# Optimization experiments

Hardware: AMD Instinct MI355X
Metric: run time of the kernel (lower is better)

Reference implementation:

```python
import jax, jax.numpy as jnp
import numpy as np

N = 100000   # nodes
E = 400000   # edges
B = 4000     # graphs
D = 300      # emb_dim
L = 5        # num_layer
MAX_LEN = 50 # max_atom_num (hard-coded in forward)
SELF_LOOP_BOND_TYPE = 4
BN_EPS = 1e-5


def setup_inputs() -> dict:
    key = jax.random.key(0)
    ks = jax.random.split(key, 12)
    x = jax.random.randint(ks[0], (N, 2), 0, 3)            # col0 atom type (<120), col1 chirality (<3)
    edge_index = jax.random.randint(ks[1], (2, E), 0, N)
    edge_attr = jax.random.randint(ks[2], (E, 2), 0, 3)    # col0 bond type (<6), col1 direction (<3)
    batch = jnp.sort(jax.random.randint(ks[3], (N,), 0, B))
    sc = 0.05
    x_emb1 = jax.random.normal(ks[4], (120, D)) * sc
    x_emb2 = jax.random.normal(ks[5], (3, D)) * sc
    e_emb1 = jax.random.normal(ks[6], (L, 6, D)) * sc
    e_emb2 = jax.random.normal(ks[7], (L, 3, D)) * sc
    W1 = jax.random.normal(ks[8], (L, D, 2 * D)) * (1.0 / np.sqrt(D))
    b1 = jnp.zeros((L, 2 * D))
    W2 = jax.random.normal(ks[9], (L, 2 * D, D)) * (1.0 / np.sqrt(2 * D))
    b2 = jnp.zeros((L, D))
    bn_gamma = jnp.ones((L, D))
    bn_beta = jnp.zeros((L, D))
    return dict(x=x, edge_index=edge_index, edge_attr=edge_attr, batch=batch,
                num_graphs=B, x_emb1=x_emb1, x_emb2=x_emb2, e_emb1=e_emb1,
                e_emb2=e_emb2, W1=W1, b1=b1, W2=W2, b2=b2,
                bn_gamma=bn_gamma, bn_beta=bn_beta)


def reference(x, edge_index, edge_attr, batch, num_graphs,
              x_emb1, x_emb2, e_emb1, e_emb2, W1, b1, W2, b2, bn_gamma, bn_beta):
    n = x.shape[0]
    # input node embedding: atom type + chirality
    h = x_emb1[x[:, 0]] + x_emb2[x[:, 1]]  # [N, D]
    # add self loops (bond_type=4, direction=0)
    loop = jnp.arange(n)
    src = jnp.concatenate([edge_index[0], loop])
    dst = jnp.concatenate([edge_index[1], loop])
    ea0 = jnp.concatenate([edge_attr[:, 0], jnp.full((n,), SELF_LOOP_BOND_TYPE, edge_attr.dtype)])
    ea1 = jnp.concatenate([edge_attr[:, 1], jnp.zeros((n,), edge_attr.dtype)])
    num_layers = W1.shape[0]
    for l in range(num_layers):
        ee = e_emb1[l][ea0] + e_emb2[l][ea1]                 # [E+N, D] edge embeddings
        msg = h[src] + ee                                     # gather + message
        agg = jax.ops.segment_sum(msg, dst, num_segments=n)   # scatter-add aggregation
        hid = jax.nn.relu(agg @ W1[l] + b1[l])                # GIN MLP
        h2 = hid @ W2[l] + b2[l]
        mean = h2.mean(axis=0)                                # BatchNorm1d (batch stats, biased var)
        var = jnp.mean((h2 - mean) ** 2, axis=0)
        h2 = (h2 - mean) * jax.lax.rsqrt(var + BN_EPS) * bn_gamma[l] + bn_beta[l]
        # dropout with drop_ratio=0 is identity; relu on all but last layer
        h = h2 if l == num_layers - 1 else jax.nn.relu(h2)
    # global mean pool over graphs
    counts = jax.ops.segment_sum(jnp.ones((n,), h.dtype), batch, num_segments=num_graphs)
    pooled = jax.ops.segment_sum(h, batch, num_segments=num_graphs) / jnp.maximum(counts, 1.0)[:, None]
    # atom_feature_pad: pad per-graph node features to MAX_LEN with mask
    idx = jnp.arange(n)
    is_start = jnp.concatenate([jnp.array([True]), batch[1:] != batch[:-1]])
    start = jax.lax.cummax(jnp.where(is_start, idx, 0))
    pos = idx - start                                          # position within each graph
    valid = pos < MAX_LEN
    posc = jnp.minimum(pos, MAX_LEN - 1)
    d = h.shape[1]
    node_feature = jnp.zeros((num_graphs, MAX_LEN, d), h.dtype).at[batch, posc].add(
        h * valid[:, None].astype(h.dtype))
    mask = jnp.zeros((num_graphs, MAX_LEN), h.dtype).at[batch, posc].add(valid.astype(h.dtype))
    return pooled, node_feature, mask
```

## Files before the change

### kernel.cpp

```cpp
#include <hip/hip_runtime.h>
#include <cstdint>

#define D 300
#define MAXLEN 50
#define K1P 320
#define H1 600
#define H1P 608
#define W1ROWS 640
#define W2ROWS 384

typedef __attribute__((ext_vector_type(8))) short s16x8;
typedef __attribute__((ext_vector_type(4))) short s16x4;
typedef __attribute__((ext_vector_type(4))) float f32x4;
typedef __attribute__((ext_vector_type(2))) float f32x2;
typedef __attribute__((ext_vector_type(4))) int i32x4;

__device__ __forceinline__ unsigned short f2b(float f) {
  uint32_t u = __builtin_bit_cast(uint32_t, f);
  u += 0x7FFFu + ((u >> 16) & 1u);
  return (unsigned short)(u >> 16);
}
__device__ __forceinline__ float b2f(unsigned short s) {
  return __builtin_bit_cast(float, (uint32_t)s << 16);
}
__device__ __forceinline__ void gld_lds16(const void* g, void* l) {
  __builtin_amdgcn_global_load_lds((const __attribute__((address_space(1))) void*)g,
                                   (__attribute__((address_space(3))) void*)l, 16, 0, 0);
}

__global__ void k_cmb(const float* __restrict__ xe1, const float* __restrict__ xe2,
                      unsigned short* __restrict__ cmb, int total ) {
  int i = blockIdx.x * blockDim.x + threadIdx.x;
  if (i >= total) return;
  int c = i / 75, d = (i - c * 75) * 4;
  int a = c / 3, b = c - a * 3;
  s16x4 out;
#pragma unroll
  for (int j = 0; j < 4; ++j) out[j] = (short)f2b(xe1[(size_t)a * D + d + j] + xe2[(size_t)b * D + d + j]);
  *(s16x4*)(cmb + (size_t)c * K1P + d) = out;
}

__global__ void k_cid(const int* __restrict__ x, int* __restrict__ cid, int N) {
  int i = blockIdx.x * blockDim.x + threadIdx.x;
  if (i < N) cid[i] = x[2 * i] * 3 + x[2 * i + 1];
}

__global__ void k_count(const int* __restrict__ key, int* __restrict__ cnt, int n) {
  int i = blockIdx.x * blockDim.x + threadIdx.x;
  if (i < n) atomicAdd(&cnt[key[i]], 1);
}

__global__ void k_scan1(const int* __restrict__ in, int* __restrict__ part, int n) {
  __shared__ int red[256];
  int tid = threadIdx.x;
  int base = blockIdx.x * 1024 + tid * 4;
  i32x4 v = {0, 0, 0, 0};
  if (base + 3 < n) v = *(const i32x4*)(in + base);
  else {
#pragma unroll
    for (int k = 0; k < 4; ++k) v[k] = (base + k < n) ? in[base + k] : 0;
  }
  int s = v[0] + v[1] + v[2] + v[3];
  red[tid] = s;
  __syncthreads();
  for (int off = 1; off < 256; off <<= 1) {
    int t = (tid >= off) ? red[tid - off] : 0;
    __syncthreads();
    red[tid] += t;
    __syncthreads();
  }
  if (tid == 255) part[blockIdx.x] = red[255];
}

__global__ void k_scan2(int* __restrict__ part, int P) {
  __shared__ int sm[1024];
  int tid = threadIdx.x;
  int v = (tid < P) ? part[tid] : 0;
  sm[tid] = v;
  __syncthreads();
  for (int off = 1; off < 1024; off <<= 1) {
    int t = (tid >= off) ? sm[tid - off] : 0;
    __syncthreads();
    sm[tid] += t;
    __syncthreads();
  }
  if (tid < P) part[tid] = sm[tid] - v;
  if (tid == 1023) part[P] = sm[1023];
}

__global__ void k_scan3(const int* __restrict__ in, const int* __restrict__ part,
                        int* __restrict__ out, int n, int P) {
  __shared__ int red[256];
  int tid = threadIdx.x;
  int base = blockIdx.x * 1024 + tid * 4;
  i32x4 v = {0, 0, 0, 0};
  if (base + 3 < n) v = *(const i32x4*)(in + base);
  else {
#pragma unroll
    for (int k = 0; k < 4; ++k) v[k] = (base + k < n) ? in[base + k] : 0;
  }
  int s = v[0] + v[1] + v[2] + v[3];
  red[tid] = s;
  __syncthreads();
  for (int off = 1; off < 256; off <<= 1) {
    int t = (tid >= off) ? red[tid - off] : 0;
    __syncthreads();
    red[tid] += t;
    __syncthreads();
  }
  int pre = red[tid] - s + part[blockIdx.x];
  if (base < n) out[base] = pre;
  if (base + 1 < n) out[base + 1] = pre + v[0];
  if (base + 2 < n) out[base + 2] = pre + v[0] + v[1];
  if (base + 3 < n) out[base + 3] = pre + v[0] + v[1] + v[2];
  if (blockIdx.x == 0 && tid == 0) out[n] = part[P];
}

__global__ void k_fill(const int* __restrict__ src, const int* __restrict__ dst,
                       const int* __restrict__ ea, const int* __restrict__ cid,
                       int* __restrict__ cur, const int* __restrict__ offs,
                       int* __restrict__ ssrc, int* __restrict__ scid,
                       int* __restrict__ cnt18, int E_) {
  int e = blockIdx.x * blockDim.x + threadIdx.x;
  if (e >= E_) return;
  int d = dst[e];
  int s = src[e];
  int p = atomicAdd(&cur[d], 1);
  int pos = offs[d] + p;
  ssrc[pos] = s;
  scid[pos] = cid[s];
  int co = ea[2 * e] * 3 + ea[2 * e + 1];
  atomicAdd(&cnt18[d * 18 + co], 1);
}

__global__ void k_cnt18bf(const int* __restrict__ cnt18, unsigned short* __restrict__ aggbf, int N) {
  int idx = blockIdx.x * blockDim.x + threadIdx.x;
  if (idx >= N * 10) return;
  int i = idx / 10, j = idx - i * 10;
  uint32_t o = 0;
  if (j < 9) {
    int c0 = cnt18[i * 18 + 2 * j] + (2 * j == 12 ? 1 : 0);
    int c1 = cnt18[i * 18 + 2 * j + 1];
    o = (uint32_t)f2b((float)c0) | ((uint32_t)f2b((float)c1) << 16);
  }
  *(uint32_t*)(aggbf + (size_t)i * K1P + D + j * 2) = o;
}

__global__ void k_ecw1(const float* __restrict__ ee1, const float* __restrict__ ee2,
                       const float* __restrict__ W1, unsigned short* __restrict__ W1tA,
                       int L_, int total ) {
  int idx = blockIdx.x * blockDim.x + threadIdx.x;
  if (idx >= total) return;
  int k18 = idx % 18;
  int n = (idx / 18) % H1;
  int l = idx / (18 * H1);
  const float* e1 = ee1 + ((size_t)l * 6 + k18 / 3) * D;
  const float* e2 = ee2 + ((size_t)l * 3 + k18 % 3) * D;
  const float* w = W1 + (size_t)l * D * H1 + n;
  float s = 0.f;
  for (int d = 0; d < D; ++d) s += (e1[d] + e2[d]) * w[(size_t)d * H1];
  W1tA[(size_t)l * W1ROWS * K1P + (size_t)n * K1P + D + k18] = f2b(s);
}

template <int FUSE>
__global__ void k_agg(const unsigned short* __restrict__ hin, const int* __restrict__ ridx,
                      const int* __restrict__ offs, const float* __restrict__ scale,
                      const float* __restrict__ shift, const int* __restrict__ selfcid,
                      unsigned short* __restrict__ aggbf, int N) {
  int w = (int)((blockIdx.x * blockDim.x + threadIdx.x) >> 6);
  if (w >= N) return;
  int lane = threadIdx.x & 63;
  float sc0[3], sc1[3], sh0[3], sh1[3];
#pragma unroll
  for (int i = 0; i < 3; ++i) {
    int d2 = i * 64 + lane;
    if (FUSE && d2 < 150) {
      f32x2 s = *(const f32x2*)(scale + d2 * 2);
      f32x2 t = *(const f32x2*)(shift + d2 * 2);
      sc0[i] = s[0]; sc1[i] = s[1]; sh0[i] = t[0]; sh1[i] = t[1];
    } else { sc0[i] = sc1[i] = sh0[i] = sh1[i] = 0.f; }
  }
  int beg = offs[w], end = offs[w + 1];
  int wrow = FUSE ? w : selfcid[w];
  float s0[3], s1[3];
#pragma unroll
  for (int i = 0; i < 3; ++i) {
    int d2 = i * 64 + lane;
    float a = 0.f, b = 0.f;
    if (d2 < 150) {
      uint32_t u = *(const uint32_t*)(hin + (size_t)wrow * K1P + d2 * 2);
      a = b2f((unsigned short)(u & 0xFFFF));
      b = b2f((unsigned short)(u >> 16));
      if (FUSE) { a = fmaxf(a * sc0[i] + sh0[i], 0.f); b = fmaxf(b * sc1[i] + sh1[i], 0.f); }
    }
    s0[i] = a; s1[i] = b;
  }
  int j = beg;
  for (; j + 4 <= end; j += 4) {
    int sv0 = ridx[j], sv1 = ridx[j + 1], sv2 = ridx[j + 2], sv3 = ridx[j + 3];
    const unsigned short* p0 = hin + (size_t)sv0 * K1P;
    const unsigned short* p1 = hin + (size_t)sv1 * K1P;
    const unsigned short* p2 = hin + (size_t)sv2 * K1P;
    const unsigned short* p3 = hin + (size_t)sv3 * K1P;
#pragma unroll
    for (int i = 0; i < 3; ++i) {
      int d2 = i * 64 + lane;
      if (d2 < 150) {
        uint32_t u0 = *(const uint32_t*)(p0 + d2 * 2);
        uint32_t u1 = *(const uint32_t*)(p1 + d2 * 2);
        uint32_t u2 = *(const uint32_t*)(p2 + d2 * 2);
        uint32_t u3 = *(const uint32_t*)(p3 + d2 * 2);
        float a0 = b2f((unsigned short)(u0 & 0xFFFF)), b0 = b2f((unsigned short)(u0 >> 16));
        float a1 = b2f((unsigned short)(u1 & 0xFFFF)), b1 = b2f((unsigned short)(u1 >> 16));
        float a2 = b2f((unsigned short)(u2 & 0xFFFF)), b2 = b2f((unsigned short)(u2 >> 16));
        float a3 = b2f((unsigned short)(u3 & 0xFFFF)), b3 = b2f((unsigned short)(u3 >> 16));
        if (FUSE) {
          a0 = fmaxf(a0 * sc0[i] + sh0[i], 0.f); b0 = fmaxf(b0 * sc1[i] + sh1[i], 0.f);
          a1 = fmaxf(a1 * sc0[i] + sh0[i], 0.f); b1 = fmaxf(b1 * sc1[i] + sh1[i], 0.f);
          a2 = fmaxf(a2 * sc0[i] + sh0[i], 0.f); b2 = fmaxf(b2 * sc1[i] + sh1[i], 0.f);
          a3 = fmaxf(a3 * sc0[i] + sh0[i], 0.f); b3 = fmaxf(b3 * sc1[i] + sh1[i], 0.f);
        }
        s0[i] += (a0 + a1) + (a2 + a3);
        s1[i] += (b0 + b1) + (b2 + b3);
      }
    }
  }
  for (; j < end; ++j) {
    int sv = ridx[j];
    const unsigned short* rp = hin + (size_t)sv * K1P;
#pragma unroll
    for (int i = 0; i < 3; ++i) {
      int d2 = i * 64 + lane;
      if (d2 < 150) {
        uint32_t u = *(const uint32_t*)(rp + d2 * 2);
        float a = b2f((unsigned short)(u & 0xFFFF)), b = b2f((unsigned short)(u >> 16));
        if (FUSE) { a = fmaxf(a * sc0[i] + sh0[i], 0.f); b = fmaxf(b * sc1[i] + sh1[i], 0.f); }
        s0[i] += a;
        s1[i] += b;
      }
    }
  }
#pragma unroll
  for (int i = 0; i < 3; ++i) {
    int d2 = i * 64 + lane;
    if (d2 < 150) {
      uint32_t o = (uint32_t)f2b(s0[i]) | ((uint32_t)f2b(s1[i]) << 16);
      *(uint32_t*)(aggbf + (size_t)w * K1P + d2 * 2) = o;
    }
  }
}

__global__ void k_wconv(const float* __restrict__ W, unsigned short* __restrict__ Wt,
                        int K, int Nout, int Kp, int total) {
  int idx = blockIdx.x * blockDim.x + threadIdx.x;
  if (idx >= total) return;
  int n = idx / Kp, k = idx - n * Kp;
  float v = (k < K && n < Nout) ? W[(size_t)k * Nout + n] : 0.f;
  Wt[idx] = f2b(v);
}

template <int K, int EPI>
__global__ __launch_bounds__(256, 3) void k_gemm(
    const unsigned short* __restrict__ A, const unsigned short* __restrict__ Bt,
    const float* __restrict__ bias, unsigned short* __restrict__ Cb,
    float* __restrict__ sums, int M, int Nout, int ldc, int CT) {
  constexpr int T = K / 32;
  __shared__ __align__(16) unsigned short smem[24576];

  int nwg = gridDim.x;
  int q = nwg >> 3, r8 = nwg & 7;
  int xcd = blockIdx.x & 7, oidx = blockIdx.x >> 3;
  int wid = (xcd < r8 ? xcd * (q + 1) : r8 * (q + 1) + (xcd - r8) * q) + oidx;
  int ct = wid % CT, rt = wid / CT;
  const int rowBase = rt * 128, colBase = ct * 128;

  const int tid = threadIdx.x, lane = tid & 63, wave = tid >> 6;
  const int wm = wave >> 1, wn = wave & 1;
  const int l15 = lane & 15, lg = lane >> 4;

  unsigned short* Asm = smem;
  unsigned short* Bsm = smem + 12288;

  auto stage = [&](int s, int t) {
#pragma unroll
    for (int i = 0; i < 2; ++i) {
      int u = tid + i * 256;
      int rr = u >> 2;
      int cdat = (u & 3) ^ ((rr >> 1) & 3);
      int gr = rowBase + rr; if (gr >= M) gr = M - 1;
      gld_lds16(A + (size_t)gr * K + t * 32 + cdat * 8, Asm + s * 4096 + u * 8);
      gld_lds16(Bt + (size_t)(colBase + rr) * K + t * 32 + cdat * 8, Bsm + s * 4096 + u * 8);
    }
  };

  f32x4 acc[4][4] = {};
  stage(0, 0);
  stage(1, 1);
#pragma unroll
  for (int t = 0; t < T; ++t) {
    if (t + 1 < T) asm volatile("s_waitcnt vmcnt(4)" ::: "memory");
    else           asm volatile("s_waitcnt vmcnt(0)" ::: "memory");
    __builtin_amdgcn_s_barrier();
    __builtin_amdgcn_sched_barrier(0);
    const unsigned short* bA = Asm + (t % 3) * 4096;
    const unsigned short* bB = Bsm + (t % 3) * 4096;
    s16x8 af[4], bf[4];
#pragma unroll
    for (int i = 0; i < 4; ++i) {
      int ra = wm * 64 + i * 16 + l15;
      int rb = wn * 64 + i * 16 + l15;
      af[i] = *(const s16x8*)(bA + ((size_t)ra * 4 + (lg ^ ((ra >> 1) & 3))) * 8);
      bf[i] = *(const s16x8*)(bB + ((size_t)rb * 4 + (lg ^ ((rb >> 1) & 3))) * 8);
    }
    if (t + 2 < T) stage((t + 2) % 3, t + 2);
#pragma unroll
    for (int mi = 0; mi < 4; ++mi)
#pragma unroll
      for (int ni = 0; ni < 4; ++ni)
        acc[mi][ni] = __builtin_amdgcn_mfma_f32_16x16x32_bf16(af[mi], bf[ni], acc[mi][ni], 0, 0, 0);
  }

  float bnS[4] = {0.f, 0.f, 0.f, 0.f}, bnQ[4] = {0.f, 0.f, 0.f, 0.f};
#pragma unroll
  for (int ni = 0; ni < 4; ++ni) {
    int col = colBase + wn * 64 + ni * 16 + l15;
    if (col >= (EPI ? ldc : Nout)) continue;
    bool inN = col < Nout;
    float bv = inN ? bias[col] : 0.f;
#pragma unroll
    for (int mi = 0; mi < 4; ++mi) {
      int row0 = rowBase + wm * 64 + mi * 16 + lg * 4;
#pragma unroll
      for (int rr = 0; rr < 4; ++rr) {
        int row = row0 + rr;
        if (row < M) {
          float v = inN ? acc[mi][ni][rr] + bv : 0.f;
          if (EPI) v = fmaxf(v, 0.f);
          else { bnS[ni] += v; bnQ[ni] += v * v; }
          Cb[(size_t)row * ldc + col] = f2b(v);
        }
      }
    }
  }
  if (!EPI) {
#pragma unroll
    for (int ni = 0; ni < 4; ++ni) {
      float cs = bnS[ni], cq = bnQ[ni];
      cs += __shfl_xor(cs, 16); cq += __shfl_xor(cq, 16);
      cs += __shfl_xor(cs, 32); cq += __shfl_xor(cq, 32);
      int col = colBase + wn * 64 + ni * 16 + l15;
      if (lg == 0 && col < Nout) {
        atomicAdd(&sums[col], cs);
        atomicAdd(&sums[D + col], cq);
      }
    }
  }
}

__global__ void k_bnfinal(const float* __restrict__ sums, const float* __restrict__ sumsq,
                          const float* __restrict__ gamma, const float* __restrict__ beta,
                          float* __restrict__ scale, float* __restrict__ shift, int N) {
  int c = threadIdx.x;
  if (c >= D) return;
  float inv = 1.f / (float)N;
  float mean = sums[c] * inv;
  float var = sumsq[c] * inv - mean * mean;
  if (var < 0.f) var = 0.f;
  float sc = gamma[c] * rsqrtf(var + 1e-5f);
  scale[c] = sc;
  shift[c] = beta[c] - mean * sc;
}

__global__ void k_pool(const unsigned short* __restrict__ hb, const float* __restrict__ scale,
                       const float* __restrict__ shift, const int* __restrict__ gs,
                       const int* __restrict__ gc, float* __restrict__ pooled, int total ) {
  int gid = blockIdx.x * blockDim.x + threadIdx.x;
  if (gid >= total) return;
  int g = gid / 75, c4 = (gid - g * 75) * 4;
  int start = gs[g], cnt = gc[g];
  f32x4 s = {0.f, 0.f, 0.f, 0.f};
  for (int i = 0; i < cnt; ++i) {
    s16x4 in = *(const s16x4*)(hb + (size_t)(start + i) * K1P + c4);
#pragma unroll
    for (int j = 0; j < 4; ++j) s[j] += b2f((unsigned short)in[j]);
  }
  f32x4 sc = *(const f32x4*)(scale + c4);
  f32x4 sh = *(const f32x4*)(shift + c4);
  float dv = (cnt > 0) ? (float)cnt : 1.f;
  f32x4 out;
#pragma unroll
  for (int j = 0; j < 4; ++j) out[j] = (s[j] * sc[j] + sh[j] * (float)cnt) / dv;
  *(f32x4*)(pooled + (size_t)g * D + c4) = out;
}

__global__ void k_nf(const unsigned short* __restrict__ hb, const float* __restrict__ scale,
                     const float* __restrict__ shift, const int* __restrict__ gs,
                     const int* __restrict__ gc, float* __restrict__ nf, float* __restrict__ mask) {
  int g = blockIdx.x;
  int start = gs[g], cnt = gc[g];
  int lim = cnt < MAXLEN ? cnt : MAXLEN;
  for (int idx = threadIdx.x; idx < MAXLEN * 75; idx += 256) {
    int p = idx / 75;
    int c4 = (idx - p * 75) * 4;
    f32x4 v = {0.f, 0.f, 0.f, 0.f};
    if (p < lim) {
      s16x4 in = *(const s16x4*)(hb + (size_t)(start + p) * K1P + c4);
      f32x4 sc = *(const f32x4*)(scale + c4);
      f32x4 sh = *(const f32x4*)(shift + c4);
#pragma unroll
      for (int j = 0; j < 4; ++j) v[j] = b2f((unsigned short)in[j]) * sc[j] + sh[j];
    }
    *(f32x4*)(nf + (size_t)g * (MAXLEN * D) + p * D + c4) = v;
  }
  if (threadIdx.x < MAXLEN) mask[(size_t)g * MAXLEN + threadIdx.x] = (threadIdx.x < lim) ? 1.f : 0.f;
}

extern "C" void kernel_launch(void* const* d_in, const int* in_sizes, int n_in,
                              void* d_out, int out_size, void* d_ws, size_t ws_size,
                              hipStream_t stream) {
  const int* x      = (const int*)d_in[0];
  const int* ei     = (const int*)d_in[1];
  const int* ea     = (const int*)d_in[2];
  const int* batch  = (const int*)d_in[3];
  const float* xe1  = (const float*)d_in[5];
  const float* xe2  = (const float*)d_in[6];
  const float* ee1  = (const float*)d_in[7];
  const float* ee2  = (const float*)d_in[8];
  const float* W1   = (const float*)d_in[9];
  const float* b1   = (const float*)d_in[10];
  const float* W2   = (const float*)d_in[11];
  const float* b2   = (const float*)d_in[12];
  const float* gamma = (const float*)d_in[13];
  const float* beta  = (const float*)d_in[14];

  const int N = in_sizes[0] / 2;
  const int E = in_sizes[1] / 2;
  const int L = in_sizes[9] / (D * 2 * D);
  const int B = out_size / (D + MAXLEN * D + MAXLEN);

  char* ws = (char*)d_ws;
  size_t off = 0;
  auto alloc = [&](size_t bytes) -> void* {
    void* p = ws + off;
    off += (bytes + 255) & ~(size_t)255;
    return p;
  };
  unsigned short* aggbf = (unsigned short*)alloc((size_t)N * K1P * 2);
  unsigned short* hb    = (unsigned short*)alloc((size_t)N * K1P * 2);
  unsigned short* hid   = (unsigned short*)alloc((size_t)N * H1P * 2);
  unsigned short* cmb   = (unsigned short*)alloc((size_t)360 * K1P * 2);
  unsigned short* W1tA = (unsigned short*)alloc((size_t)L * W1ROWS * K1P * 2);
  unsigned short* W2tA = (unsigned short*)alloc((size_t)L * W2ROWS * H1P * 2);
  int* cnt    = (int*)alloc((size_t)N * 4);
  int* cur    = (int*)alloc((size_t)N * 4);
  int* offs   = (int*)alloc((size_t)(N + 1) * 4);
  int* cid    = (int*)alloc((size_t)N * 4);
  int* cnt18  = (int*)alloc((size_t)N * 18 * 4);
  int* ssrc   = (int*)alloc((size_t)E * 4);
  int* scid   = (int*)alloc((size_t)E * 4);
  int* gc     = (int*)alloc((size_t)B * 4);
  int* gs     = (int*)alloc((size_t)(B + 1) * 4);
  int* part   = (int*)alloc(1024 * 4);
  float* sumsA = (float*)alloc((size_t)L * 2 * D * 4);
  float* scale = (float*)alloc(2 * D * 4);

  hipMemsetAsync(cnt, 0, (size_t)N * 4, stream);
  hipMemsetAsync(cur, 0, (size_t)N * 4, stream);
  hipMemsetAsync(gc, 0, (size_t)B * 4, stream);
  hipMemsetAsync(cnt18, 0, (size_t)N * 18 * 4, stream);
  hipMemsetAsync(sumsA, 0, (size_t)L * 2 * D * 4, stream);

  k_cmb<<<(360 * 75 + 255) / 256, 256, 0, stream>>>(xe1, xe2, cmb, 360 * 75);
  k_cid<<<(N + 255) / 256, 256, 0, stream>>>(x, cid, N);
  k_count<<<(E + 255) / 256, 256, 0, stream>>>(ei + E, cnt, E);
  {
    int P = (N + 1023) / 1024;
    k_scan1<<<P, 256, 0, stream>>>(cnt, part, N);
    k_scan2<<<1, 1024, 0, stream>>>(part, P);
    k_scan3<<<P, 256, 0, stream>>>(cnt, part, offs, N, P);
  }
  k_fill<<<(E + 255) / 256, 256, 0, stream>>>(ei, ei + E, ea, cid, cur, offs, ssrc, scid, cnt18, E);
  k_cnt18bf<<<(N * 10 + 255) / 256, 256, 0, stream>>>(cnt18, aggbf, N);
  k_count<<<(N + 255) / 256, 256, 0, stream>>>(batch, gc, N);
  {
    int P = (B + 1023) / 1024;
    k_scan1<<<P, 256, 0, stream>>>(gc, part, B);
    k_scan2<<<1, 1024, 0, stream>>>(part, P);
    k_scan3<<<P, 256, 0, stream>>>(gc, part, gs, B, P);
  }
  for (int l = 0; l < L; ++l) {
    k_wconv<<<(W1ROWS * K1P + 255) / 256, 256, 0, stream>>>(
        W1 + (size_t)l * D * H1, W1tA + (size_t)l * W1ROWS * K1P, D, H1, K1P, W1ROWS * K1P);
    k_wconv<<<(W2ROWS * H1P + 255) / 256, 256, 0, stream>>>(
        W2 + (size_t)l * H1 * D, W2tA + (size_t)l * W2ROWS * H1P, H1, D, H1P, W2ROWS * H1P);
  }
  k_ecw1<<<(L * H1 * 18 + 255) / 256, 256, 0, stream>>>(ee1, ee2, W1, W1tA, L, L * H1 * 18);

  const int RT = (N + 127) / 128;
  for (int l = 0; l < L; ++l) {
    float* sums = sumsA + (size_t)l * 2 * D;
    if (l == 0)
      k_agg<0><<<(N + 3) / 4, 256, 0, stream>>>(cmb, scid, offs, nullptr, nullptr, cid, aggbf, N);
    else
      k_agg<1><<<(N + 3) / 4, 256, 0, stream>>>(hb, ssrc, offs, scale, scale + D, nullptr, aggbf, N);
    k_gemm<K1P, 1><<<5 * RT, 256, 0, stream>>>(
        aggbf, W1tA + (size_t)l * W1ROWS * K1P, b1 + (size_t)l * H1, hid, nullptr, N, H1, H1P, 5);
    k_gemm<H1P, 0><<<3 * RT, 256, 0, stream>>>(
        hid, W2tA + (size_t)l * W2ROWS * H1P, b2 + (size_t)l * D, hb, sums, N, D, K1P, 3);
    k_bnfinal<<<1, 320, 0, stream>>>(sums, sums + D, gamma + (size_t)l * D, beta + (size_t)l * D,
                                     scale, scale + D, N);
  }

  float* out = (float*)d_out;
  float* out_pooled = out;
  float* out_nf = out + (size_t)B * D;
  float* out_mask = out + (size_t)B * D + (size_t)B * MAXLEN * D;
  k_pool<<<(B * 75 + 255) / 256, 256, 0, stream>>>(hb, scale, scale + D, gs, gc, out_pooled, B * 75);
  k_nf<<<B, 256, 0, stream>>>(hb, scale, scale + D, gs, gc, out_nf, out_mask);
}
```

Before: 1.673 ms.

## Load GEMM A operand directly into registers, stage only B through LDS

The A tile is no longer staged through shared memory. Each lane loads its MFMA A fragments straight from global memory into a double-buffered register set, prefetched two k-steps ahead. Only the B tile stays in the three-stage LDS pipeline, which halves LDS use, and the launch bounds move from 3 to 4 waves per SIMD to raise occupancy. The cost is more vector registers, direct global loads that are less coalesced and not shared across waves, and the A prefetch for step t+2 now issues after the MFMAs instead of before them.

Result: slower. 2.589 ms (+54.7%).

```diff
diff --git a/kernel.cpp b/kernel.cpp
--- a/kernel.cpp
+++ b/kernel.cpp
@@ -260,12 +260,12 @@
 }
 
 template <int K, int EPI>
-__global__ __launch_bounds__(256, 3) void k_gemm(
+__global__ __launch_bounds__(256, 4) void k_gemm(
     const unsigned short* __restrict__ A, const unsigned short* __restrict__ Bt,
     const float* __restrict__ bias, unsigned short* __restrict__ Cb,
     float* __restrict__ sums, int M, int Nout, int ldc, int CT) {
   constexpr int T = K / 32;
-  __shared__ __align__(16) unsigned short smem[24576];
+  __shared__ __align__(16) unsigned short Bsm[3 * 4096];
 
   int nwg = gridDim.x;
   int q = nwg >> 3, r8 = nwg & 7;
@@ -278,46 +278,56 @@
   const int wm = wave >> 1, wn = wave & 1;
   const int l15 = lane & 15, lg = lane >> 4;
 
-  unsigned short* Asm = smem;
-  unsigned short* Bsm = smem + 12288;
-
-  auto stage = [&](int s, int t) {
+  const unsigned short* Arow[4];
+#pragma unroll
+  for (int mi = 0; mi < 4; ++mi) {
+    int r = rowBase + wm * 64 + mi * 16 + l15;
+    if (r >= M) r = M - 1;
+    Arow[mi] = A + (size_t)r * K + lg * 8;
+  }
+
+  auto stageB = [&](int s, int t) {
 #pragma unroll
     for (int i = 0; i < 2; ++i) {
       int u = tid + i * 256;
       int rr = u >> 2;
       int cdat = (u & 3) ^ ((rr >> 1) & 3);
-      int gr = rowBase + rr; if (gr >= M) gr = M - 1;
-      gld_lds16(A + (size_t)gr * K + t * 32 + cdat * 8, Asm + s * 4096 + u * 8);
       gld_lds16(Bt + (size_t)(colBase + rr) * K + t * 32 + cdat * 8, Bsm + s * 4096 + u * 8);
     }
   };
 
+  s16x8 aset[2][4];
+#pragma unroll
+  for (int mi = 0; mi < 4; ++mi) aset[0][mi] = *(const s16x8*)(Arow[mi]);
+  stageB(0, 0);
+#pragma unroll
+  for (int mi = 0; mi < 4; ++mi) aset[1][mi] = *(const s16x8*)(Arow[mi] + 32);
+  stageB(1, 1);
+
   f32x4 acc[4][4] = {};
-  stage(0, 0);
-  stage(1, 1);
 #pragma unroll
   for (int t = 0; t < T; ++t) {
-    if (t + 1 < T) asm volatile("s_waitcnt vmcnt(4)" ::: "memory");
+    if (t + 1 < T) asm volatile("s_waitcnt vmcnt(6)" ::: "memory");
     else           asm volatile("s_waitcnt vmcnt(0)" ::: "memory");
     __builtin_amdgcn_s_barrier();
     __builtin_amdgcn_sched_barrier(0);
-    const unsigned short* bA = Asm + (t % 3) * 4096;
     const unsigned short* bB = Bsm + (t % 3) * 4096;
-    s16x8 af[4], bf[4];
+    s16x8 bf[4];
 #pragma unroll
     for (int i = 0; i < 4; ++i) {
-      int ra = wm * 64 + i * 16 + l15;
       int rb = wn * 64 + i * 16 + l15;
-      af[i] = *(const s16x8*)(bA + ((size_t)ra * 4 + (lg ^ ((ra >> 1) & 3))) * 8);
       bf[i] = *(const s16x8*)(bB + ((size_t)rb * 4 + (lg ^ ((rb >> 1) & 3))) * 8);
     }
-    if (t + 2 < T) stage((t + 2) % 3, t + 2);
 #pragma unroll
     for (int mi = 0; mi < 4; ++mi)
 #pragma unroll
       for (int ni = 0; ni < 4; ++ni)
-        acc[mi][ni] = __builtin_amdgcn_mfma_f32_16x16x32_bf16(af[mi], bf[ni], acc[mi][ni], 0, 0, 0);
+        acc[mi][ni] = __builtin_amdgcn_mfma_f32_16x16x32_bf16(aset[t & 1][mi], bf[ni], acc[mi][ni], 0, 0, 0);
+    if (t + 2 < T) {
+#pragma unroll
+      for (int mi = 0; mi < 4; ++mi) aset[t & 1][mi] = *(const s16x8*)(Arow[mi] + (t + 2) * 32);
+      stageB((t + 2) % 3, t + 2);
+    }
   }
 
   float bnS[4] = {0.f, 0.f, 0.f, 0.f}, bnQ[4] = {0.f, 0.f, 0.f, 0.f};
```
